# Kernel optimization log

Measured on AMD Instinct MI355X. Metric: run time of the kernel, lower is better.

## Reference

```python
import jax, jax.numpy as jnp
import numpy as np

N = 10000
E = 160000
IN_C = 512
OUT_C = 1024
NEG_SLOPE = 0.2


def setup_inputs() -> dict:
    key = jax.random.key(0)
    ks = jax.random.split(key, 12)
    x = jax.random.normal(ks[0], (N, IN_C), dtype=jnp.float32)
    edge_index = jax.random.randint(ks[1], (2, E), 0, N, dtype=jnp.int32)
    s_in = 1.0 / np.sqrt(IN_C)
    s_out = 1.0 / np.sqrt(OUT_C)
    return {
        "x": x,
        "edge_index": edge_index,
        "W1": jax.random.normal(ks[2], (IN_C, OUT_C), dtype=jnp.float32) * s_in,
        "a_src1": jax.random.normal(ks[3], (OUT_C,), dtype=jnp.float32) * s_out,
        "a_dst1": jax.random.normal(ks[4], (OUT_C,), dtype=jnp.float32) * s_out,
        "b1": jnp.zeros((OUT_C,), dtype=jnp.float32),
        "W2": jax.random.normal(ks[5], (IN_C, OUT_C), dtype=jnp.float32) * s_in,
        "a_src2": jax.random.normal(ks[6], (OUT_C,), dtype=jnp.float32) * s_out,
        "a_dst2": jax.random.normal(ks[7], (OUT_C,), dtype=jnp.float32) * s_out,
        "b2": jnp.zeros((OUT_C,), dtype=jnp.float32),
        "prelu_a": jnp.asarray(0.25, dtype=jnp.float32),
        "Wp1": jax.random.normal(ks[8], (OUT_C, OUT_C), dtype=jnp.float32) * s_out,
        "bp1": jnp.zeros((OUT_C,), dtype=jnp.float32),
        "Wp2": jax.random.normal(ks[9], (OUT_C, 1024), dtype=jnp.float32) * s_out,
    }


def _gat_conv(x, src, dst, W, a_src, a_dst, b):
    # x: [N, in], W: [in, out]. PyG GATConv, heads=1, self-loops already in src/dst.
    h = x @ W  # [N, out]
    alpha_s = h @ a_src  # [N]
    alpha_d = h @ a_dst  # [N]
    e = alpha_s[src] + alpha_d[dst]  # [E+N]
    e = jnp.where(e >= 0, e, NEG_SLOPE * e)  # LeakyReLU(0.2)
    # segment softmax over destination nodes
    m = jax.ops.segment_max(e, dst, num_segments=N)  # [N]
    ex = jnp.exp(e - m[dst])
    denom = jax.ops.segment_sum(ex, dst, num_segments=N)  # [N], >=1 via self-loops
    alpha = ex / denom[dst]  # [E+N]
    out = jax.ops.segment_sum(alpha[:, None] * h[src], dst, num_segments=N)
    return out + b


def reference(x, edge_index, W1, a_src1, a_dst1, b1, W2, a_src2, a_dst2, b2,
              prelu_a, Wp1, bp1, Wp2):
    # add self loops (PyG GATConv default)
    loops = jnp.arange(N, dtype=edge_index.dtype)
    src = jnp.concatenate([edge_index[0], loops])
    dst = jnp.concatenate([edge_index[1], loops])

    def prelu(v):
        return jnp.where(v >= 0, v, prelu_a * v)

    h1 = prelu(_gat_conv(x, src, dst, W1, a_src1, a_dst1, b1))  # [N, 1024]
    h2 = prelu(_gat_conv(x, src, dst, W2, a_src2, a_dst2, b2))  # [N, 1024]
    h = h1 + h2

    # semantic attention: project -> mean over nodes -> softmax over 1024 dims
    w = jnp.tanh(h @ Wp1 + bp1) @ Wp2  # [N, 1024]
    w = w.mean(axis=0)  # [1024]
    att = jax.nn.softmax(w, axis=0)  # [1024] == beta.mean(0).squeeze()
    return att * h1 + (1.0 - att) * h2
```

## Files before the change

### kernel.cpp

```cpp
#include <hip/hip_runtime.h>

#define IN_C 512
#define OUT_C 1024
#define NC2 2048
#define NEG_SLOPE 0.2f

typedef short frag8 __attribute__((ext_vector_type(8)));
typedef float f32x4 __attribute__((ext_vector_type(4)));

#define GLOAD_LDS16(g, l) __builtin_amdgcn_global_load_lds(\
    (const __attribute__((address_space(1))) void*)(g), \
    (__attribute__((address_space(3))) void*)(l), 16, 0, 0)

__device__ __forceinline__ unsigned short f2b(float f){
  unsigned u = __float_as_uint(f);
  unsigned r = (u + 0x7fffu + ((u >> 16) & 1u)) >> 16;
  return (unsigned short)r;
}
__device__ __forceinline__ unsigned encf(float f){
  unsigned u = __float_as_uint(f);
  return (u & 0x80000000u) ? ~u : (u | 0x80000000u);
}
__device__ __forceinline__ float decf(unsigned u){
  unsigned v = (u & 0x80000000u) ? (u & 0x7fffffffu) : ~u;
  return __uint_as_float(v);
}
__device__ __forceinline__ float leaky(float v){ return v >= 0.f ? v : NEG_SLOPE * v; }


__global__ void prep_kernel(const float* __restrict__ W1, const float* __restrict__ W2,
                            const float* __restrict__ Wp1,
                            const float* __restrict__ a_src1, const float* __restrict__ a_dst1,
                            const float* __restrict__ a_src2, const float* __restrict__ a_dst2,
                            unsigned short* __restrict__ WT, unsigned short* __restrict__ Wp1T,
                            float* __restrict__ uv){
  __shared__ float tile[32][33];
  int b = blockIdx.x;
  int tx = threadIdx.x & 31, ty = threadIdx.x >> 5;
  if (b < 1024){
    const float* in = (b >> 9) ? W2 : W1;
    int rowOff = (b >> 9) * OUT_C;
    int bb = b & 511;
    int c0 = (bb & 31) * 32, r0 = (bb >> 5) * 32;
    for (int i = ty; i < 32; i += 8)
      tile[i][tx] = in[(size_t)(r0 + i) * OUT_C + c0 + tx];
    __syncthreads();
    for (int i = ty; i < 32; i += 8)
      WT[(size_t)(c0 + i + rowOff) * IN_C + r0 + tx] = f2b(tile[tx][i]);
  } else if (b < 2048){
    int bb = b - 1024;
    int c0 = (bb & 31) * 32, r0 = (bb >> 5) * 32;
    for (int i = ty; i < 32; i += 8)
      tile[i][tx] = Wp1[(size_t)(r0 + i) * OUT_C + c0 + tx];
    __syncthreads();
    for (int i = ty; i < 32; i += 8)
      Wp1T[(size_t)(c0 + i) * OUT_C + r0 + tx] = f2b(tile[tx][i]);
  } else {
    int g = (b - 2048) * 4 + (threadIdx.x >> 6);
    int lane = threadIdx.x & 63;
    int which = g >> 9;
    int i = g & 511;
    const float* W = (which < 2) ? W1 : W2;
    const float* a = (which == 0) ? a_src1 : (which == 1) ? a_dst1 : (which == 2) ? a_src2 : a_dst2;
    const float* row = W + (size_t)i * OUT_C;
    float s = 0.f;
    for (int j = lane; j < OUT_C; j += 64) s += row[j] * a[j];
    for (int off = 32; off; off >>= 1) s += __shfl_down(s, off);
    if (lane == 0) uv[which * IN_C + i] = s;
  }
}


__global__ void alpha_kernel(const float* __restrict__ x, const float* __restrict__ uv,
                             unsigned short* __restrict__ xb,
                             float* __restrict__ as1, float* __restrict__ ad1,
                             float* __restrict__ as2, float* __restrict__ ad2,
                             float* __restrict__ self1, float* __restrict__ self2,
                             unsigned* __restrict__ m1e, unsigned* __restrict__ m2e,
                             int* counts, int* cursor, float* colsum, float* wv){
  int n = blockIdx.x;
  int w = threadIdx.x >> 6, lane = threadIdx.x & 63;
  __shared__ float sh[4];
  if (threadIdx.x == 0){ counts[n] = 0; cursor[n] = 0; }
  if (n < 8){
    int i = n * 256 + threadIdx.x;
    if (i < 1024) colsum[i] = 0.f; else wv[i - 1024] = 0.f;
  }
  const float* row = x + (size_t)n * IN_C;
  const float* u = uv + w * IN_C;
  float s = 0.f;
  for (int j = lane; j < IN_C; j += 64){
    float v = row[j];
    s += v * u[j];
    if (w == 0) xb[(size_t)n * IN_C + j] = f2b(v);
  }
  for (int off = 32; off; off >>= 1) s += __shfl_down(s, off);
  if (lane == 0){
    sh[w] = s;
    if (w == 0) as1[n] = s;
    else if (w == 1) ad1[n] = s;
    else if (w == 2) as2[n] = s;
    else ad2[n] = s;
  }
  __syncthreads();
  if (threadIdx.x == 0){
    float e1 = leaky(sh[0] + sh[1]);
    float e2 = leaky(sh[2] + sh[3]);
    self1[n] = e1; self2[n] = e2;
    m1e[n] = encf(e1); m2e[n] = encf(e2);
  }
}


__global__ void histmax_kernel(const int* __restrict__ src, const int* __restrict__ dst,
                               const float* __restrict__ as1, const float* __restrict__ ad1,
                               const float* __restrict__ as2, const float* __restrict__ ad2,
                               int* counts, unsigned* m1e, unsigned* m2e, int E){
  int e = blockIdx.x * 256 + threadIdx.x;
  if (e >= E) return;
  int s = src[e], d = dst[e];
  atomicAdd(&counts[d], 1);
  atomicMax(&m1e[d], encf(leaky(as1[s] + ad1[d])));
  atomicMax(&m2e[d], encf(leaky(as2[s] + ad2[d])));
}

__global__ void scanA_kernel(const int* __restrict__ counts, int* __restrict__ offs,
                             int* __restrict__ bsum, int n){
  __shared__ int wsum[4];
  int i = blockIdx.x * 256 + threadIdx.x;
  int wave = threadIdx.x >> 6, lane = threadIdx.x & 63;
  int v = (i < n) ? counts[i] : 0;
  int sc = v;
  for (int o = 1; o < 64; o <<= 1){
    int t = __shfl_up(sc, o);
    if (lane >= o) sc += t;
  }
  if (lane == 63) wsum[wave] = sc;
  __syncthreads();
  int wp = 0, tot = 0;
#pragma unroll
  for (int k = 0; k < 4; k++){
    int ws = wsum[k];
    if (k < wave) wp += ws;
    tot += ws;
  }
  if (i < n) offs[i] = wp + sc - v;
  if (threadIdx.x == 0) bsum[blockIdx.x] = tot;
}

__global__ void scanB_kernel(int* __restrict__ bsum, int nb){
  int lane = threadIdx.x;
  int v = (lane < nb) ? bsum[lane] : 0;
  int sc = v;
  for (int o = 1; o < 64; o <<= 1){
    int t = __shfl_up(sc, o);
    if (lane >= o) sc += t;
  }
  if (lane < nb) bsum[lane] = sc - v;
}

__global__ void scanC_kernel(int* __restrict__ offs, const int* __restrict__ bsum, int n){
  int i = blockIdx.x * 256 + threadIdx.x;
  if (i < n) offs[i] += bsum[blockIdx.x];
}

__global__ void denominit_kernel(const unsigned* __restrict__ m1e, const unsigned* __restrict__ m2e,
                                 const float* __restrict__ self1, const float* __restrict__ self2,
                                 float* __restrict__ m1, float* __restrict__ m2,
                                 float* __restrict__ den1, float* __restrict__ den2, int N){
  int i = blockIdx.x * 256 + threadIdx.x;
  if (i >= N) return;
  float a = decf(m1e[i]), b = decf(m2e[i]);
  m1[i] = a; m2[i] = b;
  den1[i] = expf(self1[i] - a);
  den2[i] = expf(self2[i] - b);
}

__global__ void scatterexp_kernel(const int* __restrict__ src, const int* __restrict__ dst,
                                  const int* __restrict__ offs, int* cursor,
                                  const float* __restrict__ as1, const float* __restrict__ ad1,
                                  const float* __restrict__ as2, const float* __restrict__ ad2,
                                  const float* __restrict__ m1, const float* __restrict__ m2,
                                  int* __restrict__ nsrc, float* __restrict__ nw1, float* __restrict__ nw2,
                                  float* den1, float* den2, int E){
  int e = blockIdx.x * 256 + threadIdx.x;
  if (e >= E) return;
  int s = src[e], d = dst[e];
  int p = atomicAdd(&cursor[d], 1);
  int idx = offs[d] + p;
  float x1 = expf(leaky(as1[s] + ad1[d]) - m1[d]);
  float x2 = expf(leaky(as2[s] + ad2[d]) - m2[d]);
  nsrc[idx] = s; nw1[idx] = x1; nw2[idx] = x2;
  atomicAdd(&den1[d], x1);
  atomicAdd(&den2[d], x2);
}


#define AGG_FMA8(ACC, W, U) \
  ACC[0] += (W) * __uint_as_float(((unsigned)(U).x) << 16); \
  ACC[1] += (W) * __uint_as_float(((unsigned)(U).x) & 0xffff0000u); \
  ACC[2] += (W) * __uint_as_float(((unsigned)(U).y) << 16); \
  ACC[3] += (W) * __uint_as_float(((unsigned)(U).y) & 0xffff0000u); \
  ACC[4] += (W) * __uint_as_float(((unsigned)(U).z) << 16); \
  ACC[5] += (W) * __uint_as_float(((unsigned)(U).z) & 0xffff0000u); \
  ACC[6] += (W) * __uint_as_float(((unsigned)(U).w) << 16); \
  ACC[7] += (W) * __uint_as_float(((unsigned)(U).w) & 0xffff0000u);

__global__ __launch_bounds__(256) void aggx_kernel(
    const int* __restrict__ counts, const int* __restrict__ offs,
    const int* __restrict__ nsrc, const float* __restrict__ nw1, const float* __restrict__ nw2,
    const float* __restrict__ den1, const float* __restrict__ den2,
    const float* __restrict__ self1, const float* __restrict__ self2,
    const float* __restrict__ m1, const float* __restrict__ m2,
    const unsigned short* __restrict__ xb,
    unsigned short* __restrict__ xa1b, unsigned short* __restrict__ xa2b, int N){
  int tid = threadIdx.x;
  int g = tid >> 4, hl = tid & 15;
  int grpbase = tid & 48;
  int d = blockIdx.y * 16 + g;
  if (d >= N) return;
  int colbase = blockIdx.x * 128 + hl * 8;
  float inv1 = 1.f / den1[d], inv2 = 1.f / den2[d];
  int deg = counts[d], off = offs[d];
  float acc1[8] = {0,0,0,0,0,0,0,0}, acc2[8] = {0,0,0,0,0,0,0,0};
  const unsigned short* Xb = xb + colbase;
  for (int base = 0; base < deg; base += 16){
    int i = base + hl;
    int s = 0; float w1 = 0.f, w2 = 0.f;
    if (i < deg){
      int p = off + i;
      s = nsrc[p];
      w1 = nw1[p] * inv1;
      w2 = nw2[p] * inv2;
    }
    int cnt = min(16, deg - base);
#pragma unroll 4
    for (int j = 0; j < cnt; j++){
      int sj = __shfl(s, grpbase + j);
      float w1j = __shfl(w1, grpbase + j);
      float w2j = __shfl(w2, grpbase + j);
      int4 u = *(const int4*)(Xb + (size_t)sj * IN_C);
      AGG_FMA8(acc1, w1j, u)
      AGG_FMA8(acc2, w2j, u)
    }
  }
  {
    float ws1 = expf(self1[d] - m1[d]) * inv1;
    float ws2 = expf(self2[d] - m2[d]) * inv2;
    int4 u = *(const int4*)(Xb + (size_t)d * IN_C);
    AGG_FMA8(acc1, ws1, u)
    AGG_FMA8(acc2, ws2, u)
  }
  size_t outb = (size_t)d * IN_C + colbase;
  int4 o1, o2;
  o1.x = (int)((unsigned)f2b(acc1[0]) | ((unsigned)f2b(acc1[1]) << 16));
  o1.y = (int)((unsigned)f2b(acc1[2]) | ((unsigned)f2b(acc1[3]) << 16));
  o1.z = (int)((unsigned)f2b(acc1[4]) | ((unsigned)f2b(acc1[5]) << 16));
  o1.w = (int)((unsigned)f2b(acc1[6]) | ((unsigned)f2b(acc1[7]) << 16));
  o2.x = (int)((unsigned)f2b(acc2[0]) | ((unsigned)f2b(acc2[1]) << 16));
  o2.y = (int)((unsigned)f2b(acc2[2]) | ((unsigned)f2b(acc2[3]) << 16));
  o2.z = (int)((unsigned)f2b(acc2[4]) | ((unsigned)f2b(acc2[5]) << 16));
  o2.w = (int)((unsigned)f2b(acc2[6]) | ((unsigned)f2b(acc2[7]) << 16));
  *(int4*)(xa1b + outb) = o1;
  *(int4*)(xa2b + outb) = o2;
}


__global__ __launch_bounds__(256) void gemmh_kernel(const unsigned short* __restrict__ A1,
                                                    const unsigned short* __restrict__ A2,
                                                    const unsigned short* __restrict__ BT,
                                                    const float* __restrict__ b1,
                                                    const float* __restrict__ b2,
                                                    const float* __restrict__ prelu_a,
                                                    unsigned short* __restrict__ hsum,
                                                    unsigned short* __restrict__ hdiff,
                                                    int M, int Mtiles, int perx){
  const int bid = blockIdx.x;
  const int xcd = bid & 7;
  const int li = bid >> 3;
  const int bn_t = li & 7;
  const int bm_t = xcd * perx + (li >> 3);
  if (bm_t >= Mtiles) return;
  const int bm = bm_t * 64, bn = bn_t * 128;
  __shared__ unsigned short Al[64 * 32];
  __shared__ unsigned short Bl[128 * 32];
  const int t = threadIdx.x;
  const int lane = t & 63, wid = t >> 6;
  const int wj = wid;
  const int l16 = lane & 15, q = lane >> 4;
  const int lch = (lane & 3) * 8;
  f32x4 acc1[4][2] = {};
  f32x4 acc2[4][2] = {};
  const int arow = bm + wid * 16 + (lane >> 2);
  const int brow0 = bn + wid * 32 + (lane >> 2);
  const int ga = min(arow, M - 1);
  const unsigned short* pa1 = A1 + (size_t)ga * IN_C + lch;
  const unsigned short* pa2 = A2 + (size_t)ga * IN_C + lch;
  const unsigned short* pb0 = BT + (size_t)brow0 * IN_C + lch;
  const unsigned short* pb1 = BT + (size_t)(brow0 + 16) * IN_C + lch;
  const size_t boff2 = (size_t)OUT_C * IN_C;
  for (int k0 = 0; k0 < IN_C; k0 += 32){
    GLOAD_LDS16(pa1 + k0, &Al[(wid * 16) * 32]);
    GLOAD_LDS16(pb0 + k0, &Bl[(wid * 32) * 32]);
    GLOAD_LDS16(pb1 + k0, &Bl[(wid * 32 + 16) * 32]);
    __syncthreads();
    frag8 af[4], bf[2];
#pragma unroll
    for (int mi = 0; mi < 4; mi++) af[mi] = *(const frag8*)&Al[(mi*16 + l16) * 32 + q*8];
#pragma unroll
    for (int nj = 0; nj < 2; nj++) bf[nj] = *(const frag8*)&Bl[(wj*32 + nj*16 + l16) * 32 + q*8];
#pragma unroll
    for (int mi = 0; mi < 4; mi++)
#pragma unroll
      for (int nj = 0; nj < 2; nj++)
        acc1[mi][nj] = __builtin_amdgcn_mfma_f32_16x16x32_bf16(af[mi], bf[nj], acc1[mi][nj], 0, 0, 0);
    __syncthreads();
  }
  for (int k0 = 0; k0 < IN_C; k0 += 32){
    GLOAD_LDS16(pa2 + k0, &Al[(wid * 16) * 32]);
    GLOAD_LDS16(pb0 + boff2 + k0, &Bl[(wid * 32) * 32]);
    GLOAD_LDS16(pb1 + boff2 + k0, &Bl[(wid * 32 + 16) * 32]);
    __syncthreads();
    frag8 af[4], bf[2];
#pragma unroll
    for (int mi = 0; mi < 4; mi++) af[mi] = *(const frag8*)&Al[(mi*16 + l16) * 32 + q*8];
#pragma unroll
    for (int nj = 0; nj < 2; nj++) bf[nj] = *(const frag8*)&Bl[(wj*32 + nj*16 + l16) * 32 + q*8];
#pragma unroll
    for (int mi = 0; mi < 4; mi++)
#pragma unroll
      for (int nj = 0; nj < 2; nj++)
        acc2[mi][nj] = __builtin_amdgcn_mfma_f32_16x16x32_bf16(af[mi], bf[nj], acc2[mi][nj], 0, 0, 0);
    __syncthreads();
  }
  float pa = prelu_a[0];
#pragma unroll
  for (int mi = 0; mi < 4; mi++){
#pragma unroll
    for (int r = 0; r < 4; r++){
      int row = bm + mi*16 + q*4 + r;
      if (row >= M) continue;
#pragma unroll
      for (int nj = 0; nj < 2; nj++){
        int col = bn + wj*32 + nj*16 + l16;
        float v1 = acc1[mi][nj][r] + b1[col];
        v1 = v1 >= 0.f ? v1 : pa * v1;
        float v2 = acc2[mi][nj][r] + b2[col];
        v2 = v2 >= 0.f ? v2 : pa * v2;
        size_t idx = (size_t)row * OUT_C + col;
        hsum[idx]  = f2b(v1 + v2);
        hdiff[idx] = f2b(v1 - v2);
      }
    }
  }
}


__global__ __launch_bounds__(256) void gemm2_kernel(const unsigned short* __restrict__ A,
                                                    const unsigned short* __restrict__ BT,
                                                    const float* __restrict__ bp1,
                                                    float* __restrict__ colsum,
                                                    int M, int Mtiles, int perx){
  const int bid = blockIdx.x;
  const int xcd = bid & 7;
  const int li = bid >> 3;
  const int bn_t = li & 7;
  const int bm_t = xcd * perx + (li >> 3);
  if (bm_t >= Mtiles) return;
  const int bm = bm_t * 64, bn = bn_t * 128;
  __shared__ unsigned short Al[64 * 32];
  __shared__ unsigned short Bl[128 * 32];
  __shared__ float cs[128];
  const int t = threadIdx.x;
  const int lane = t & 63, wid = t >> 6;
  const int wj = wid;
  const int l16 = lane & 15, q = lane >> 4;
  const int lch = (lane & 3) * 8;
  if (t < 128) cs[t] = 0.f;
  f32x4 acc[4][2] = {};
  const int arow = bm + wid * 16 + (lane >> 2);
  const int brow0 = bn + wid * 32 + (lane >> 2);
  const int ga = min(arow, M - 1);
  const unsigned short* pa = A + (size_t)ga * OUT_C + lch;
  const unsigned short* pb0 = BT + (size_t)brow0 * OUT_C + lch;
  const unsigned short* pb1 = BT + (size_t)(brow0 + 16) * OUT_C + lch;
  for (int k0 = 0; k0 < OUT_C; k0 += 32){
    GLOAD_LDS16(pa + k0, &Al[(wid * 16) * 32]);
    GLOAD_LDS16(pb0 + k0, &Bl[(wid * 32) * 32]);
    GLOAD_LDS16(pb1 + k0, &Bl[(wid * 32 + 16) * 32]);
    __syncthreads();
    frag8 af[4], bf[2];
#pragma unroll
    for (int mi = 0; mi < 4; mi++) af[mi] = *(const frag8*)&Al[(mi*16 + l16) * 32 + q*8];
#pragma unroll
    for (int nj = 0; nj < 2; nj++) bf[nj] = *(const frag8*)&Bl[(wj*32 + nj*16 + l16) * 32 + q*8];
#pragma unroll
    for (int mi = 0; mi < 4; mi++)
#pragma unroll
      for (int nj = 0; nj < 2; nj++)
        acc[mi][nj] = __builtin_amdgcn_mfma_f32_16x16x32_bf16(af[mi], bf[nj], acc[mi][nj], 0, 0, 0);
    __syncthreads();
  }
#pragma unroll
  for (int nj = 0; nj < 2; nj++){
    int col = bn + wj*32 + nj*16 + l16;
    float bias = bp1[col];
    float p = 0.f;
#pragma unroll
    for (int mi = 0; mi < 4; mi++){
#pragma unroll
      for (int r = 0; r < 4; r++){
        int row = bm + mi*16 + q*4 + r;
        float tv = tanhf(acc[mi][nj][r] + bias);
        if (row < M) p += tv;
      }
    }
    p += __shfl_xor(p, 16);
    p += __shfl_xor(p, 32);
    if (q == 0) atomicAdd(&cs[wj*32 + nj*16 + l16], p);
  }
  __syncthreads();
  if (t < 128) atomicAdd(&colsum[bn + t], cs[t]);
}


__global__ void wproj_kernel(const float* __restrict__ colsum, const float* __restrict__ Wp2,
                             float* __restrict__ wv){
  int o = blockIdx.x * 256 + threadIdx.x;
  int c0 = blockIdx.y * 128;
  float acc = 0.f;
  for (int c = c0; c < c0 + 128; c++) acc += colsum[c] * Wp2[(size_t)c * OUT_C + o];
  atomicAdd(&wv[o], acc);
}

__global__ __launch_bounds__(1024) void softmax_kernel(const float* __restrict__ wv,
                                                       float* __restrict__ att, float invN){
  int o = threadIdx.x;
  __shared__ float red[1024];
  float w = wv[o] * invN;
  red[o] = w; __syncthreads();
  for (int s = 512; s > 0; s >>= 1){ if (o < s) red[o] = fmaxf(red[o], red[o + s]); __syncthreads(); }
  float m = red[0]; __syncthreads();
  float e = expf(w - m);
  red[o] = e; __syncthreads();
  for (int s = 512; s > 0; s >>= 1){ if (o < s) red[o] += red[o + s]; __syncthreads(); }
  att[o] = e / red[0];
}

__global__ void combine_kernel(const float* __restrict__ att, const unsigned short* __restrict__ hs,
                               const unsigned short* __restrict__ hd, float* __restrict__ out, int total8){
  int i = blockIdx.x * 256 + threadIdx.x;
  if (i >= total8) return;
  int colb = (i & 127) * 8;
  int4 us = ((const int4*)hs)[i];
  int4 ud = ((const int4*)hd)[i];
  float4 a0 = *(const float4*)(att + colb);
  float4 a1 = *(const float4*)(att + colb + 4);
  float o[8]; float sv, dv;
  sv = __uint_as_float(((unsigned)us.x) << 16);        dv = __uint_as_float(((unsigned)ud.x) << 16);
  o[0] = 0.5f * sv + (a0.x - 0.5f) * dv;
  sv = __uint_as_float(((unsigned)us.x) & 0xffff0000u); dv = __uint_as_float(((unsigned)ud.x) & 0xffff0000u);
  o[1] = 0.5f * sv + (a0.y - 0.5f) * dv;
  sv = __uint_as_float(((unsigned)us.y) << 16);        dv = __uint_as_float(((unsigned)ud.y) << 16);
  o[2] = 0.5f * sv + (a0.z - 0.5f) * dv;
  sv = __uint_as_float(((unsigned)us.y) & 0xffff0000u); dv = __uint_as_float(((unsigned)ud.y) & 0xffff0000u);
  o[3] = 0.5f * sv + (a0.w - 0.5f) * dv;
  sv = __uint_as_float(((unsigned)us.z) << 16);        dv = __uint_as_float(((unsigned)ud.z) << 16);
  o[4] = 0.5f * sv + (a1.x - 0.5f) * dv;
  sv = __uint_as_float(((unsigned)us.z) & 0xffff0000u); dv = __uint_as_float(((unsigned)ud.z) & 0xffff0000u);
  o[5] = 0.5f * sv + (a1.y - 0.5f) * dv;
  sv = __uint_as_float(((unsigned)us.w) << 16);        dv = __uint_as_float(((unsigned)ud.w) << 16);
  o[6] = 0.5f * sv + (a1.z - 0.5f) * dv;
  sv = __uint_as_float(((unsigned)us.w) & 0xffff0000u); dv = __uint_as_float(((unsigned)ud.w) & 0xffff0000u);
  o[7] = 0.5f * sv + (a1.w - 0.5f) * dv;
  float4 f0; f0.x = o[0]; f0.y = o[1]; f0.z = o[2]; f0.w = o[3];
  float4 f1; f1.x = o[4]; f1.y = o[5]; f1.z = o[6]; f1.w = o[7];
  *(float4*)(out + (size_t)i * 8) = f0;
  *(float4*)(out + (size_t)i * 8 + 4) = f1;
}


extern "C" void kernel_launch(void* const* d_in, const int* in_sizes, int n_in,
                              void* d_out, int out_size, void* d_ws, size_t ws_size,
                              hipStream_t stream){
  const float* x      = (const float*)d_in[0];
  const int*   edge   = (const int*)d_in[1];
  const float* W1     = (const float*)d_in[2];
  const float* a_src1 = (const float*)d_in[3];
  const float* a_dst1 = (const float*)d_in[4];
  const float* b1     = (const float*)d_in[5];
  const float* W2     = (const float*)d_in[6];
  const float* a_src2 = (const float*)d_in[7];
  const float* a_dst2 = (const float*)d_in[8];
  const float* b2     = (const float*)d_in[9];
  const float* prelu_a= (const float*)d_in[10];
  const float* Wp1    = (const float*)d_in[11];
  const float* bp1    = (const float*)d_in[12];
  const float* Wp2    = (const float*)d_in[13];
  const int N = in_sizes[0] / IN_C;
  const int E = in_sizes[1] / 2;
  const int* srcArr = edge;
  const int* dstArr = edge + E;

  char* ws = (char*)d_ws;
  size_t o = 0;
  auto alloc = [&](size_t b) -> char* {
    char* p = ws + o;
    o = (o + b + 255) & ~(size_t)255;
    return p;
  };
  unsigned short* xb    = (unsigned short*)alloc((size_t)N * IN_C * 2);
  unsigned short* WT    = (unsigned short*)alloc((size_t)NC2 * IN_C * 2);
  unsigned short* Wp1T  = (unsigned short*)alloc((size_t)OUT_C * OUT_C * 2);
  unsigned short* xa1b  = (unsigned short*)alloc((size_t)N * IN_C * 2);
  unsigned short* xa2b  = (unsigned short*)alloc((size_t)N * IN_C * 2);
  unsigned short* hsum  = (unsigned short*)alloc((size_t)N * OUT_C * 2);
  unsigned short* hdiff = (unsigned short*)alloc((size_t)N * OUT_C * 2);
  float*          uv    = (float*)alloc(4 * IN_C * 4);
  float*          as1   = (float*)alloc((size_t)4 * N * 4);
  float* ad1 = as1 + N; float* as2 = as1 + 2 * N; float* ad2 = as1 + 3 * N;
  float*          self1 = (float*)alloc((size_t)2 * N * 4); float* self2 = self1 + N;
  unsigned*       m1e   = (unsigned*)alloc((size_t)2 * N * 4); unsigned* m2e = m1e + N;
  float*          m1    = (float*)alloc((size_t)2 * N * 4); float* m2 = m1 + N;
  float*          den1  = (float*)alloc((size_t)2 * N * 4); float* den2 = den1 + N;
  int*            counts= (int*)alloc((size_t)N * 4);
  int*            offs  = (int*)alloc((size_t)(N + 1) * 4);
  int*            cursor= (int*)alloc((size_t)N * 4);
  int*            bsum  = (int*)alloc(64 * 4);
  int*            nsrc  = (int*)alloc((size_t)E * 4);
  float*          nw1   = (float*)alloc((size_t)E * 4);
  float*          nw2   = (float*)alloc((size_t)E * 4);
  float*          colsum= (float*)alloc(OUT_C * 4);
  float*          wv    = (float*)alloc(OUT_C * 4);
  float*          att   = (float*)alloc(OUT_C * 4);

  const int Mtiles = (N + 63) / 64;
  const int perx = (Mtiles + 7) / 8;
  const int gemmgrid = 8 * perx * 8;
  const int nchunk = (N + 255) / 256;

  prep_kernel<<<2560, 256, 0, stream>>>(W1, W2, Wp1, a_src1, a_dst1, a_src2, a_dst2, WT, Wp1T, uv);
  alpha_kernel<<<N, 256, 0, stream>>>(x, uv, xb, as1, ad1, as2, ad2, self1, self2, m1e, m2e,
                                      counts, cursor, colsum, wv);
  histmax_kernel<<<(E + 255) / 256, 256, 0, stream>>>(srcArr, dstArr, as1, ad1, as2, ad2,
                                                      counts, m1e, m2e, E);
  scanA_kernel<<<nchunk, 256, 0, stream>>>(counts, offs, bsum, N);
  scanB_kernel<<<1, 64, 0, stream>>>(bsum, nchunk);
  scanC_kernel<<<nchunk, 256, 0, stream>>>(offs, bsum, N);
  denominit_kernel<<<nchunk, 256, 0, stream>>>(m1e, m2e, self1, self2, m1, m2, den1, den2, N);
  scatterexp_kernel<<<(E + 255) / 256, 256, 0, stream>>>(srcArr, dstArr, offs, cursor,
                                                         as1, ad1, as2, ad2, m1, m2,
                                                         nsrc, nw1, nw2, den1, den2, E);
  aggx_kernel<<<dim3(4, (N + 15) / 16), 256, 0, stream>>>(counts, offs, nsrc, nw1, nw2, den1, den2,
                                                          self1, self2, m1, m2, xb, xa1b, xa2b, N);
  gemmh_kernel<<<gemmgrid, 256, 0, stream>>>(xa1b, xa2b, WT, b1, b2, prelu_a,
                                             hsum, hdiff, N, Mtiles, perx);
  gemm2_kernel<<<gemmgrid, 256, 0, stream>>>(hsum, Wp1T, bp1, colsum, N, Mtiles, perx);
  wproj_kernel<<<dim3(4, 8), 256, 0, stream>>>(colsum, Wp2, wv);
  softmax_kernel<<<1, 1024, 0, stream>>>(wv, att, 1.0f / (float)N);
  combine_kernel<<<(N * OUT_C / 8 + 255) / 256, 256, 0, stream>>>(att, hsum, hdiff, (float*)d_out,
                                                                  N * OUT_C / 8);
}
```

Before: 328.3 us.

## Enlarge GEMM tiles to 128x128, double-buffer A in LDS, keep B in registers

Both MFMA GEMM kernels (gemmh and gemm2) move from 64x128 to 128x128 block tiles with a 2x2 wave layout, so each wave computes a 64x64 sub-tile. The A tile is double-buffered in LDS and the next chunk is prefetched during compute. B fragments are now loaded straight from global memory into registers with a one-step prefetch instead of being staged through LDS. This is meant to raise arithmetic intensity and overlap loads with MFMA work, at the cost of more accumulator registers, uncoalesced per-lane B loads from global, and fewer blocks to cover the GPU.

New measurement: 376.8 us. 1.15x slower.

```diff
diff --git a/kernel.cpp b/kernel.cpp
--- a/kernel.cpp
+++ b/kernel.cpp
@@ -266,83 +266,108 @@
 }
 
 
-__global__ __launch_bounds__(256) void gemmh_kernel(const unsigned short* __restrict__ A1,
-                                                    const unsigned short* __restrict__ A2,
-                                                    const unsigned short* __restrict__ BT,
-                                                    const float* __restrict__ b1,
-                                                    const float* __restrict__ b2,
-                                                    const float* __restrict__ prelu_a,
-                                                    unsigned short* __restrict__ hsum,
-                                                    unsigned short* __restrict__ hdiff,
-                                                    int M, int Mtiles, int perx){
+__global__ __launch_bounds__(256, 2) void gemmh_kernel(const unsigned short* __restrict__ A1,
+                                                       const unsigned short* __restrict__ A2,
+                                                       const unsigned short* __restrict__ BT,
+                                                       const float* __restrict__ b1,
+                                                       const float* __restrict__ b2,
+                                                       const float* __restrict__ prelu_a,
+                                                       unsigned short* __restrict__ hsum,
+                                                       unsigned short* __restrict__ hdiff,
+                                                       int M, int Mtiles, int perx){
   const int bid = blockIdx.x;
   const int xcd = bid & 7;
   const int li = bid >> 3;
   const int bn_t = li & 7;
   const int bm_t = xcd * perx + (li >> 3);
   if (bm_t >= Mtiles) return;
-  const int bm = bm_t * 64, bn = bn_t * 128;
-  __shared__ unsigned short Al[64 * 32];
-  __shared__ unsigned short Bl[128 * 32];
+  const int bm = bm_t * 128, bn = bn_t * 128;
+  __shared__ unsigned short Al[2][128 * 32];
   const int t = threadIdx.x;
   const int lane = t & 63, wid = t >> 6;
-  const int wj = wid;
+  const int wi = wid & 1, wj = wid >> 1;
   const int l16 = lane & 15, q = lane >> 4;
   const int lch = (lane & 3) * 8;
-  f32x4 acc1[4][2] = {};
-  f32x4 acc2[4][2] = {};
-  const int arow = bm + wid * 16 + (lane >> 2);
-  const int brow0 = bn + wid * 32 + (lane >> 2);
-  const int ga = min(arow, M - 1);
-  const unsigned short* pa1 = A1 + (size_t)ga * IN_C + lch;
-  const unsigned short* pa2 = A2 + (size_t)ga * IN_C + lch;
-  const unsigned short* pb0 = BT + (size_t)brow0 * IN_C + lch;
-  const unsigned short* pb1 = BT + (size_t)(brow0 + 16) * IN_C + lch;
+  const int srow = wid * 32 + (lane >> 2);
+  const int ga0 = min(bm + srow, M - 1);
+  const int ga1 = min(bm + srow + 16, M - 1);
+  const unsigned short* pa1_0 = A1 + (size_t)ga0 * IN_C + lch;
+  const unsigned short* pa1_1 = A1 + (size_t)ga1 * IN_C + lch;
+  const unsigned short* pa2_0 = A2 + (size_t)ga0 * IN_C + lch;
+  const unsigned short* pa2_1 = A2 + (size_t)ga1 * IN_C + lch;
+  const unsigned short* pb[4];
+#pragma unroll
+  for (int nj = 0; nj < 4; nj++)
+    pb[nj] = BT + (size_t)(bn + wj * 64 + nj * 16 + l16) * IN_C + q * 8;
   const size_t boff2 = (size_t)OUT_C * IN_C;
-  for (int k0 = 0; k0 < IN_C; k0 += 32){
-    GLOAD_LDS16(pa1 + k0, &Al[(wid * 16) * 32]);
-    GLOAD_LDS16(pb0 + k0, &Bl[(wid * 32) * 32]);
-    GLOAD_LDS16(pb1 + k0, &Bl[(wid * 32 + 16) * 32]);
+  f32x4 acc1[4][4] = {};
+  f32x4 acc2[4][4] = {};
+  frag8 bcur[4], bnxt[4];
+
+  GLOAD_LDS16(pa1_0, &Al[0][(wid * 32) * 32]);
+  GLOAD_LDS16(pa1_1, &Al[0][(wid * 32 + 16) * 32]);
+#pragma unroll
+  for (int nj = 0; nj < 4; nj++) bcur[nj] = *(const frag8*)(pb[nj]);
+  __syncthreads();
+#pragma unroll
+  for (int k = 0; k < 16; k++){
+    const int p = k & 1;
+    if (k < 15){
+      const int k1 = (k + 1) * 32;
+      GLOAD_LDS16(pa1_0 + k1, &Al[1 - p][(wid * 32) * 32]);
+      GLOAD_LDS16(pa1_1 + k1, &Al[1 - p][(wid * 32 + 16) * 32]);
+#pragma unroll
+      for (int nj = 0; nj < 4; nj++) bnxt[nj] = *(const frag8*)(pb[nj] + k1);
+    }
+    frag8 af[4];
+#pragma unroll
+    for (int mi = 0; mi < 4; mi++) af[mi] = *(const frag8*)&Al[p][(wi*64 + mi*16 + l16) * 32 + q*8];
+#pragma unroll
+    for (int mi = 0; mi < 4; mi++)
+#pragma unroll
+      for (int nj = 0; nj < 4; nj++)
+        acc1[mi][nj] = __builtin_amdgcn_mfma_f32_16x16x32_bf16(af[mi], bcur[nj], acc1[mi][nj], 0, 0, 0);
+#pragma unroll
+    for (int nj = 0; nj < 4; nj++) bcur[nj] = bnxt[nj];
     __syncthreads();
-    frag8 af[4], bf[2];
-#pragma unroll
-    for (int mi = 0; mi < 4; mi++) af[mi] = *(const frag8*)&Al[(mi*16 + l16) * 32 + q*8];
-#pragma unroll
-    for (int nj = 0; nj < 2; nj++) bf[nj] = *(const frag8*)&Bl[(wj*32 + nj*16 + l16) * 32 + q*8];
+  }
+  GLOAD_LDS16(pa2_0, &Al[0][(wid * 32) * 32]);
+  GLOAD_LDS16(pa2_1, &Al[0][(wid * 32 + 16) * 32]);
+#pragma unroll
+  for (int nj = 0; nj < 4; nj++) bcur[nj] = *(const frag8*)(pb[nj] + boff2);
+  __syncthreads();
+#pragma unroll
+  for (int k = 0; k < 16; k++){
+    const int p = k & 1;
+    if (k < 15){
+      const int k1 = (k + 1) * 32;
+      GLOAD_LDS16(pa2_0 + k1, &Al[1 - p][(wid * 32) * 32]);
+      GLOAD_LDS16(pa2_1 + k1, &Al[1 - p][(wid * 32 + 16) * 32]);
+#pragma unroll
+      for (int nj = 0; nj < 4; nj++) bnxt[nj] = *(const frag8*)(pb[nj] + boff2 + k1);
+    }
+    frag8 af[4];
+#pragma unroll
+    for (int mi = 0; mi < 4; mi++) af[mi] = *(const frag8*)&Al[p][(wi*64 + mi*16 + l16) * 32 + q*8];
 #pragma unroll
     for (int mi = 0; mi < 4; mi++)
 #pragma unroll
-      for (int nj = 0; nj < 2; nj++)
-        acc1[mi][nj] = __builtin_amdgcn_mfma_f32_16x16x32_bf16(af[mi], bf[nj], acc1[mi][nj], 0, 0, 0);
+      for (int nj = 0; nj < 4; nj++)
+        acc2[mi][nj] = __builtin_amdgcn_mfma_f32_16x16x32_bf16(af[mi], bcur[nj], acc2[mi][nj], 0, 0, 0);
+#pragma unroll
+    for (int nj = 0; nj < 4; nj++) bcur[nj] = bnxt[nj];
     __syncthreads();
   }
-  for (int k0 = 0; k0 < IN_C; k0 += 32){
-    GLOAD_LDS16(pa2 + k0, &Al[(wid * 16) * 32]);
-    GLOAD_LDS16(pb0 + boff2 + k0, &Bl[(wid * 32) * 32]);
-    GLOAD_LDS16(pb1 + boff2 + k0, &Bl[(wid * 32 + 16) * 32]);
-    __syncthreads();
-    frag8 af[4], bf[2];
-#pragma unroll
-    for (int mi = 0; mi < 4; mi++) af[mi] = *(const frag8*)&Al[(mi*16 + l16) * 32 + q*8];
-#pragma unroll
-    for (int nj = 0; nj < 2; nj++) bf[nj] = *(const frag8*)&Bl[(wj*32 + nj*16 + l16) * 32 + q*8];
-#pragma unroll
-    for (int mi = 0; mi < 4; mi++)
-#pragma unroll
-      for (int nj = 0; nj < 2; nj++)
-        acc2[mi][nj] = __builtin_amdgcn_mfma_f32_16x16x32_bf16(af[mi], bf[nj], acc2[mi][nj], 0, 0, 0);
-    __syncthreads();
-  }
   float pa = prelu_a[0];
 #pragma unroll
   for (int mi = 0; mi < 4; mi++){
 #pragma unroll
     for (int r = 0; r < 4; r++){
-      int row = bm + mi*16 + q*4 + r;
+      int row = bm + wi*64 + mi*16 + q*4 + r;
       if (row >= M) continue;
 #pragma unroll
-      for (int nj = 0; nj < 2; nj++){
-        int col = bn + wj*32 + nj*16 + l16;
+      for (int nj = 0; nj < 4; nj++){
+        int col = bn + wj*64 + nj*16 + l16;
         float v1 = acc1[mi][nj][r] + b1[col];
         v1 = v1 >= 0.f ? v1 : pa * v1;
         float v2 = acc2[mi][nj][r] + b2[col];
@@ -356,68 +381,81 @@
 }
 
 
-__global__ __launch_bounds__(256) void gemm2_kernel(const unsigned short* __restrict__ A,
-                                                    const unsigned short* __restrict__ BT,
-                                                    const float* __restrict__ bp1,
-                                                    float* __restrict__ colsum,
-                                                    int M, int Mtiles, int perx){
+__global__ __launch_bounds__(256, 2) void gemm2_kernel(const unsigned short* __restrict__ A,
+                                                       const unsigned short* __restrict__ BT,
+                                                       const float* __restrict__ bp1,
+                                                       float* __restrict__ colsum,
+                                                       int M, int Mtiles, int perx){
   const int bid = blockIdx.x;
   const int xcd = bid & 7;
   const int li = bid >> 3;
   const int bn_t = li & 7;
   const int bm_t = xcd * perx + (li >> 3);
   if (bm_t >= Mtiles) return;
-  const int bm = bm_t * 64, bn = bn_t * 128;
-  __shared__ unsigned short Al[64 * 32];
-  __shared__ unsigned short Bl[128 * 32];
+  const int bm = bm_t * 128, bn = bn_t * 128;
+  __shared__ unsigned short Al[2][128 * 32];
   __shared__ float cs[128];
   const int t = threadIdx.x;
   const int lane = t & 63, wid = t >> 6;
-  const int wj = wid;
+  const int wi = wid & 1, wj = wid >> 1;
   const int l16 = lane & 15, q = lane >> 4;
   const int lch = (lane & 3) * 8;
   if (t < 128) cs[t] = 0.f;
-  f32x4 acc[4][2] = {};
-  const int arow = bm + wid * 16 + (lane >> 2);
-  const int brow0 = bn + wid * 32 + (lane >> 2);
-  const int ga = min(arow, M - 1);
-  const unsigned short* pa = A + (size_t)ga * OUT_C + lch;
-  const unsigned short* pb0 = BT + (size_t)brow0 * OUT_C + lch;
-  const unsigned short* pb1 = BT + (size_t)(brow0 + 16) * OUT_C + lch;
-  for (int k0 = 0; k0 < OUT_C; k0 += 32){
-    GLOAD_LDS16(pa + k0, &Al[(wid * 16) * 32]);
-    GLOAD_LDS16(pb0 + k0, &Bl[(wid * 32) * 32]);
-    GLOAD_LDS16(pb1 + k0, &Bl[(wid * 32 + 16) * 32]);
+  const int srow = wid * 32 + (lane >> 2);
+  const int ga0 = min(bm + srow, M - 1);
+  const int ga1 = min(bm + srow + 16, M - 1);
+  const unsigned short* pa0 = A + (size_t)ga0 * OUT_C + lch;
+  const unsigned short* pa1 = A + (size_t)ga1 * OUT_C + lch;
+  const unsigned short* pb[4];
+#pragma unroll
+  for (int nj = 0; nj < 4; nj++)
+    pb[nj] = BT + (size_t)(bn + wj * 64 + nj * 16 + l16) * OUT_C + q * 8;
+  f32x4 acc[4][4] = {};
+  frag8 bcur[4], bnxt[4];
+  GLOAD_LDS16(pa0, &Al[0][(wid * 32) * 32]);
+  GLOAD_LDS16(pa1, &Al[0][(wid * 32 + 16) * 32]);
+#pragma unroll
+  for (int nj = 0; nj < 4; nj++) bcur[nj] = *(const frag8*)(pb[nj]);
+  __syncthreads();
+#pragma unroll
+  for (int k = 0; k < 32; k++){
+    const int p = k & 1;
+    if (k < 31){
+      const int k1 = (k + 1) * 32;
+      GLOAD_LDS16(pa0 + k1, &Al[1 - p][(wid * 32) * 32]);
+      GLOAD_LDS16(pa1 + k1, &Al[1 - p][(wid * 32 + 16) * 32]);
+#pragma unroll
+      for (int nj = 0; nj < 4; nj++) bnxt[nj] = *(const frag8*)(pb[nj] + k1);
+    }
+    frag8 af[4];
+#pragma unroll
+    for (int mi = 0; mi < 4; mi++) af[mi] = *(const frag8*)&Al[p][(wi*64 + mi*16 + l16) * 32 + q*8];
+#pragma unroll
+    for (int mi = 0; mi < 4; mi++)
+#pragma unroll
+      for (int nj = 0; nj < 4; nj++)
+        acc[mi][nj] = __builtin_amdgcn_mfma_f32_16x16x32_bf16(af[mi], bcur[nj], acc[mi][nj], 0, 0, 0);
+#pragma unroll
+    for (int nj = 0; nj < 4; nj++) bcur[nj] = bnxt[nj];
     __syncthreads();
-    frag8 af[4], bf[2];
-#pragma unroll
-    for (int mi = 0; mi < 4; mi++) af[mi] = *(const frag8*)&Al[(mi*16 + l16) * 32 + q*8];
-#pragma unroll
-    for (int nj = 0; nj < 2; nj++) bf[nj] = *(const frag8*)&Bl[(wj*32 + nj*16 + l16) * 32 + q*8];
-#pragma unroll
-    for (int mi = 0; mi < 4; mi++)
-#pragma unroll
-      for (int nj = 0; nj < 2; nj++)
-        acc[mi][nj] = __builtin_amdgcn_mfma_f32_16x16x32_bf16(af[mi], bf[nj], acc[mi][nj], 0, 0, 0);
-    __syncthreads();
-  }
-#pragma unroll
-  for (int nj = 0; nj < 2; nj++){
-    int col = bn + wj*32 + nj*16 + l16;
+  }
+#pragma unroll
+  for (int nj = 0; nj < 4; nj++){
+    int col = bn + wj*64 + nj*16 + l16;
     float bias = bp1[col];
     float p = 0.f;
 #pragma unroll
     for (int mi = 0; mi < 4; mi++){
 #pragma unroll
       for (int r = 0; r < 4; r++){
-        int row = bm + mi*16 + q*4 + r;
+        int row = bm + wi*64 + mi*16 + q*4 + r;
         float tv = tanhf(acc[mi][nj][r] + bias);
         if (row < M) p += tv;
       }
     }
     p += __shfl_xor(p, 16);
     p += __shfl_xor(p, 32);
-    if (q == 0) atomicAdd(&cs[wj*32 + nj*16 + l16], p);
+    if (q == 0) atomicAdd(&cs[wj*64 + nj*16 + l16], p);
   }
   __syncthreads();
   if (t < 128) atomicAdd(&colsum[bn + t], cs[t]);
@@ -534,7 +572,7 @@
   float*          wv    = (float*)alloc(OUT_C * 4);
   float*          att   = (float*)alloc(OUT_C * 4);
 
-  const int Mtiles = (N + 63) / 64;
+  const int Mtiles = (N + 127) / 128;
   const int perx = (Mtiles + 7) / 8;
   const int gemmgrid = 8 * perx * 8;
   const int nchunk = (N + 255) / 256;
```
